# Kernel optimization log

Hardware: AMD Instinct MI355X
Metric: run time of the kernel (lower is better)

Reference implementation:

```python
import jax, jax.numpy as jnp
import numpy as np

B, H, W, D = 4, 64, 64, 384
M, P = 12, 9
DH = D // M             # 32 head dim
DFF = 3 * D             # 1152 FFN hidden
N = H * W               # 4096 queries (single level)


def setup_inputs():
    key = jax.random.key(0)
    ks = jax.random.split(key, 12)
    g = lambda k, s, sc=0.02: jax.random.normal(k, s, jnp.float32) * sc
    return {
        "x": jax.random.normal(ks[0], (B, D, H, W), jnp.float32),
        "qry_masks": jnp.zeros((B, H, W), jnp.float32),
        "so_w": g(ks[1], (M * P * 2, D)), "so_b": g(ks[2], (M * P * 2,)),
        "aw_w": g(ks[3], (M * P, D)), "aw_b": g(ks[4], (M * P,)),
        "vp_w": g(ks[5], (D, D)), "vp_b": jnp.zeros((D,), jnp.float32),
        "op_w": g(ks[6], (D, D)), "op_b": jnp.zeros((D,), jnp.float32),
        "ln1_g": jnp.ones((D,), jnp.float32), "ln1_b": jnp.zeros((D,), jnp.float32),
        "w1": g(ks[7], (DFF, D)), "w2": g(ks[8], (D, DFF)),
        "ln2_g": jnp.ones((D,), jnp.float32), "ln2_b": jnp.zeros((D,), jnp.float32),
        "level_embed": g(ks[9], (1, D), 1.0),
    }


def _layernorm(x, g, b, eps=1e-5):
    mu = x.mean(-1, keepdims=True)
    v = ((x - mu) ** 2).mean(-1, keepdims=True)
    return (x - mu) * jax.lax.rsqrt(v + eps) * g + b


def _sine_pos(mask):
    # mask: [B,H,W] bool. mmdet SinePositionalEncoding(num_feats=D//2, normalize=True)
    not_mask = (~mask).astype(jnp.float32)
    y = jnp.cumsum(not_mask, 1)
    x = jnp.cumsum(not_mask, 2)
    eps, scale = 1e-6, 2.0 * np.pi
    y = y / (y[:, -1:, :] + eps) * scale
    x = x / (x[:, :, -1:] + eps) * scale
    nf = D // 2
    dim_t = 10000.0 ** (2.0 * (jnp.arange(nf) // 2).astype(jnp.float32) / nf)
    px, py = x[..., None] / dim_t, y[..., None] / dim_t

    def interleave(p):
        return jnp.stack([jnp.sin(p[..., 0::2]), jnp.cos(p[..., 1::2])], -1).reshape(p.shape[:-1] + (nf,))

    return jnp.concatenate([interleave(py), interleave(px)], -1)  # [B,H,W,D]


def _bilinear_gather(v, px, py):
    # v: [B,M,HW,DH]; px,py: [B,M,NP] pixel coords (grid_sample align_corners=False, zero pad)
    x0 = jnp.floor(px); y0 = jnp.floor(py)
    lx, ly = px - x0, py - y0
    x0i, y0i = x0.astype(jnp.int32), y0.astype(jnp.int32)
    out = jnp.zeros(v.shape[:2] + (px.shape[-1], v.shape[-1]), v.dtype)
    for dx, dy, wgt in ((0, 0, (1 - lx) * (1 - ly)), (1, 0, lx * (1 - ly)),
                        (0, 1, (1 - lx) * ly), (1, 1, lx * ly)):
        xi, yi = x0i + dx, y0i + dy
        valid = ((xi >= 0) & (xi < W) & (yi >= 0) & (yi < H)).astype(v.dtype)
        idx = jnp.clip(yi, 0, H - 1) * W + jnp.clip(xi, 0, W - 1)
        g = jnp.take_along_axis(v, idx[..., None], axis=2)  # [B,M,NP,DH]
        out = out + (wgt * valid)[..., None] * g
    return out


def _msdeform_attn(q, value_in, ref, mask_flat,
                   so_w, so_b, aw_w, aw_b, vp_w, vp_b, op_w, op_b):
    value = value_in @ vp_w.T + vp_b                      # [B,N,D]
    value = jnp.where(mask_flat[..., None], 0.0, value)
    so = (q @ so_w.T + so_b).reshape(B, N, M, P, 2)       # single level
    aw = jax.nn.softmax((q @ aw_w.T + aw_b).reshape(B, N, M, P), axis=-1)
    norm = jnp.array([W, H], jnp.float32)
    loc = ref[:, :, None, None, :] + so / norm            # [B,N,M,P,2] in [0,1]
    v = value.reshape(B, N, M, DH).transpose(0, 2, 1, 3)  # [B,M,HW,DH]
    px = (loc[..., 0] * W - 0.5).transpose(0, 2, 1, 3).reshape(B, M, N * P)
    py = (loc[..., 1] * H - 0.5).transpose(0, 2, 1, 3).reshape(B, M, N * P)
    sampled = _bilinear_gather(v, px, py).reshape(B, M, N, P, DH)
    out = jnp.einsum('bmnpd,bnmp->bnmd', sampled, aw).reshape(B, N, D)
    return out @ op_w.T + op_b


def reference(x, qry_masks, so_w, so_b, aw_w, aw_b, vp_w, vp_b, op_w, op_b,
              ln1_g, ln1_b, w1, w2, ln2_g, ln2_b, level_embed):
    mask = (qry_masks == 255.0)                           # [B,H,W] bool
    pos = _sine_pos(mask).reshape(B, N, D) + level_embed[0]
    src = x.reshape(B, D, N).transpose(0, 2, 1)           # [B,N,D]
    mask_flat = mask.reshape(B, N)
    gy, gx = jnp.meshgrid((jnp.arange(H, dtype=jnp.float32) + 0.5) / H,
                          (jnp.arange(W, dtype=jnp.float32) + 0.5) / W, indexing='ij')
    ref = jnp.stack([gx.reshape(-1), gy.reshape(-1)], -1)[None]  # [1,N,2] (x,y)
    q = src
    attn = _msdeform_attn(q + pos, q, ref, mask_flat,
                          so_w, so_b, aw_w, aw_b, vp_w, vp_b, op_w, op_b)
    q = _layernorm(q + attn, ln1_g, ln1_b)
    q = _layernorm(q + jax.nn.relu(q @ w1.T) @ w2.T, ln2_g, ln2_b)
    return q.transpose(0, 2, 1).reshape(B, D, H, W)
```

## Files before the change

kernel.cpp:

```cpp
#include <hip/hip_runtime.h>
#include <math.h>

#define Bc   4
#define Hc   64
#define Wc   64
#define Dc   384
#define Nc   4096
#define Mc   12
#define Pc   9
#define DHc  32
#define DFFc 1152
#define BNc  (Bc*Nc)

typedef __attribute__((ext_vector_type(8))) short short8;
typedef __attribute__((ext_vector_type(4))) float floatx4;

__device__ __forceinline__ ushort f2bf(float f) {
    union { float f; unsigned u; } v; v.f = f;
    unsigned r = v.u + 0x7fffu + ((v.u >> 16) & 1u);
    return (ushort)(r >> 16);
}
__device__ __forceinline__ float bf2f(ushort u) {
    union { unsigned u; float f; } v; v.u = (unsigned)u << 16; return v.f;
}

__device__ __forceinline__ void gload_lds16(const void* g, void* l) {
    __builtin_amdgcn_global_load_lds(
        (const __attribute__((address_space(1))) void*)(uintptr_t)g,
        (__attribute__((address_space(3))) void*)(uintptr_t)l,
        16, 0, 0);
}

#define SOW_N  82944
#define AWW_N  41472
#define VPW_N  147456
#define OPW_N  147456
#define W1_N   442368
#define W2_N   442368
#define WTOT   1304064

__global__ void init_kernel(const float* __restrict__ so_w,
                            const float* __restrict__ aw_w,
                            const float* __restrict__ vp_w,
                            const float* __restrict__ op_w,
                            const float* __restrict__ w1,
                            const float* __restrict__ w2,
                            const float* __restrict__ so_b,
                            const float* __restrict__ aw_b,
                            const float* __restrict__ qmask,
                            ushort* __restrict__ out,
                            float* __restrict__ bias_out,
                            float* __restrict__ cum_y,
                            float* __restrict__ cum_x) {
    int i = blockIdx.x * 256 + threadIdx.x;
    if (i < WTOT) {
        float v;
        int j = i;
        if (j < SOW_N) v = so_w[j];
        else if ((j -= SOW_N) < AWW_N) v = aw_w[j];
        else if ((j -= AWW_N) < VPW_N) v = vp_w[j];
        else if ((j -= VPW_N) < OPW_N) v = op_w[j];
        else if ((j -= OPW_N) < W1_N)  v = w1[j];
        else { j -= W1_N; v = w2[j]; }
        out[i] = f2bf(v);
        return;
    }
    int j = i - WTOT;
    if (j < 384) {
        bias_out[j] = (j < 216) ? so_b[j] : (j < 324 ? aw_b[j - 216] : 0.f);
        return;
    }
    int t = j - 384;
    if (t < Bc * Wc) {
        int b = t / Wc, w = t % Wc;
        float run = 0.f;
        for (int h = 0; h < Hc; ++h) {
            run += (qmask[(b * Hc + h) * Wc + w] == 255.0f) ? 0.f : 1.f;
            cum_y[(b * Hc + h) * Wc + w] = run;
        }
    } else if (t < Bc * Wc + Bc * Hc) {
        int t2 = t - Bc * Wc;
        int b = t2 / Hc, h = t2 % Hc;
        float run = 0.f;
        for (int w = 0; w < Wc; ++w) {
            run += (qmask[(b * Hc + h) * Wc + w] == 255.0f) ? 0.f : 1.f;
            cum_x[(b * Hc + h) * Wc + w] = run;
        }
    }
}

__global__ void transpose_pos_kernel(const float* __restrict__ x,
                                     const float* __restrict__ cum_y,
                                     const float* __restrict__ cum_x,
                                     const float* __restrict__ level_embed,
                                     ushort* __restrict__ src_bf,
                                     ushort* __restrict__ qpos_bf) {
    __shared__ float tile[32][33];
    int b  = blockIdx.z;
    int n0 = blockIdx.x * 32, d0 = blockIdx.y * 32;
    int tx = threadIdx.x, ty = threadIdx.y;
    tile[ty][tx] = x[((size_t)b * Dc + (d0 + ty)) * Nc + (n0 + tx)];
    __syncthreads();
    int n = n0 + ty, d = d0 + tx;
    float v = tile[tx][ty];
    size_t oi = ((size_t)b * Nc + n) * Dc + d;
    src_bf[oi] = f2bf(v);
    int h = n >> 6, w = n & 63;
    const float TWO_PI = 6.28318530717958647692f;
    float vy = cum_y[(b * Hc + h) * Wc + w] /
               (cum_y[(b * Hc + (Hc - 1)) * Wc + w] + 1e-6f) * TWO_PI;
    float vx = cum_x[(b * Hc + h) * Wc + w] /
               (cum_x[(b * Hc + h) * Wc + (Wc - 1)] + 1e-6f) * TWO_PI;
    int   i  = (d < 192) ? d : d - 192;
    float vv = (d < 192) ? vy : vx;
    float e   = (float)(i >> 1) * (2.0f / 192.0f);
    float idt = exp2f(e * -13.28771237954945f);
    float ang = vv * idt;
    float pe  = (i & 1) ? __cosf(ang) : __sinf(ang);
    qpos_bf[oi] = f2bf(v + pe + level_embed[d]);
}

template <int KT>
__device__ __forceinline__ void gemm_core(
        const ushort* __restrict__ A, const ushort* __restrict__ Wt,
        const float* __restrict__ bias,
        float* __restrict__ Cf, ushort* __restrict__ Cb,
        int Nout, int relu, const float* __restrict__ qmask,
        ushort* As, ushort* Bs) {
    constexpr int NCH = KT / 32;
    const int tid  = threadIdx.x;
    const int m0   = blockIdx.x * 128;
    const int n0   = blockIdx.y * 128;
    const int lane = tid & 63;
    const int wv   = tid >> 6;
    const int wr   = (wv >> 1) * 64;
    const int wc   = (wv & 1) * 64;
    const int quad = lane >> 4;
    const int lrow = lane & 15;
    const int srow = wv * 32 + (lane >> 2);
    const int scol = (lane & 3) * 8;

    floatx4 acc[4][4];
    #pragma unroll
    for (int i = 0; i < 4; ++i)
        #pragma unroll
        for (int j = 0; j < 4; ++j)
            acc[i][j] = (floatx4)(0.f);

    #pragma unroll
    for (int s = 0; s < 2; ++s) {
        gload_lds16(A  + (size_t)(m0 + srow + s * 16) * KT + scol,
                    As + wv * 1024 + s * 512);
        gload_lds16(Wt + (size_t)(n0 + srow + s * 16) * KT + scol,
                    Bs + wv * 1024 + s * 512);
    }

    for (int c = 0; c < NCH; ++c) {
        const int cur = c & 1;
        __syncthreads();
        if (c + 1 < NCH) {
            const int k0 = (c + 1) * 32;
            #pragma unroll
            for (int s = 0; s < 2; ++s) {
                gload_lds16(A  + (size_t)(m0 + srow + s * 16) * KT + k0 + scol,
                            As + (cur ^ 1) * 4096 + wv * 1024 + s * 512);
                gload_lds16(Wt + (size_t)(n0 + srow + s * 16) * KT + k0 + scol,
                            Bs + (cur ^ 1) * 4096 + wv * 1024 + s * 512);
            }
        }
        short8 afr[4], bfr[4];
        #pragma unroll
        for (int i = 0; i < 4; ++i)
            afr[i] = *(const short8*)(As + cur * 4096 +
                                      (wr + i * 16 + lrow) * 32 + quad * 8);
        #pragma unroll
        for (int j = 0; j < 4; ++j)
            bfr[j] = *(const short8*)(Bs + cur * 4096 +
                                      (wc + j * 16 + lrow) * 32 + quad * 8);
        #pragma unroll
        for (int i = 0; i < 4; ++i)
            #pragma unroll
            for (int j = 0; j < 4; ++j)
                acc[i][j] = __builtin_amdgcn_mfma_f32_16x16x32_bf16(
                    afr[i], bfr[j], acc[i][j], 0, 0, 0);
    }

    float mz[4][4];
    #pragma unroll
    for (int i = 0; i < 4; ++i)
        #pragma unroll
        for (int r = 0; r < 4; ++r) {
            int row = m0 + wr + i * 16 + quad * 4 + r;
            mz[i][r] = (qmask && qmask[row] == 255.0f) ? 0.f : 1.f;
        }

    #pragma unroll
    for (int i = 0; i < 4; ++i) {
        #pragma unroll
        for (int j = 0; j < 4; ++j) {
            int col = n0 + wc + j * 16 + lrow;
            if (col >= Nout) continue;
            float bsv = bias ? bias[col] : 0.f;
            #pragma unroll
            for (int r = 0; r < 4; ++r) {
                int row = m0 + wr + i * 16 + quad * 4 + r;
                float v = acc[i][j][r] + bsv;
                if (relu) v = fmaxf(v, 0.f);
                v *= mz[i][r];
                if (Cf) Cf[(size_t)row * Nout + col] = v;
                if (Cb) Cb[(size_t)row * Nout + col] = f2bf(v);
            }
        }
    }
}

template <int KT>
__global__ __launch_bounds__(256) void gemm_single_kernel(
        const ushort* __restrict__ A, const ushort* __restrict__ Wt,
        const float* __restrict__ bias,
        float* __restrict__ Cf, ushort* __restrict__ Cb,
        int Nout, int relu, const float* __restrict__ qmask) {
    __shared__ ushort As[2 * 128 * 32];
    __shared__ ushort Bs[2 * 128 * 32];
    gemm_core<KT>(A, Wt, bias, Cf, Cb, Nout, relu, qmask, As, Bs);
}

__global__ __launch_bounds__(256) void gemm_dual_kernel(
        const ushort* __restrict__ A0, const ushort* __restrict__ W0,
        const float* __restrict__ b0, float* __restrict__ Cf0,
        const ushort* __restrict__ A1, const ushort* __restrict__ W1,
        const float* __restrict__ b1, ushort* __restrict__ Cb1,
        const float* __restrict__ qmask) {
    __shared__ ushort As[2 * 128 * 32];
    __shared__ ushort Bs[2 * 128 * 32];
    if (blockIdx.z == 0)
        gemm_core<384>(A0, W0, b0, Cf0, nullptr, 384, 0, nullptr, As, Bs);
    else
        gemm_core<384>(A1, W1, b1, nullptr, Cb1, 384, 0, qmask, As, Bs);
}

template <int KT, int MODE>
__global__ __launch_bounds__(512, 2) void gemm_fullrow_kernel(
        const ushort* __restrict__ A, const ushort* __restrict__ Wt,
        const float* __restrict__ bias, const void* __restrict__ resid,
        const float* __restrict__ g, const float* __restrict__ beta,
        float* __restrict__ outf, ushort* __restrict__ outb) {
    constexpr int NCH = KT / 32;
    __shared__ ushort Bs[8 * 3 * 1536];
    __shared__ float eps1[8][64], eps2[8][64];
    __shared__ float mu_l[64], rs_l[64];
    const int tid  = threadIdx.x;
    const int lane = tid & 63;
    const int wv   = tid >> 6;
    const int quad = lane >> 4;
    const int lrow = lane & 15;
    const int m0   = blockIdx.x * 64;
    const int srow = lane >> 2;
    const int scol = (lane & 3) * 8;

    ushort* BsW = Bs + wv * (3 * 1536);
    const ushort* wsrc  = Wt + (size_t)(wv * 48 + srow) * KT + scol;
    const ushort* abase = A  + (size_t)(m0 + lrow) * KT + quad * 8;

    floatx4 acc[4][3];
    #pragma unroll
    for (int i = 0; i < 4; ++i)
        #pragma unroll
        for (int j = 0; j < 3; ++j)
            acc[i][j] = (floatx4)(0.f);

#define STAGE_W(c, buf)                                                      \
    gload_lds16(wsrc + (size_t)0 * 16 * KT + (c) * 32, BsW + (buf) * 1536);  \
    gload_lds16(wsrc + (size_t)1 * 16 * KT + (c) * 32, BsW + (buf) * 1536 + 512); \
    gload_lds16(wsrc + (size_t)2 * 16 * KT + (c) * 32, BsW + (buf) * 1536 + 1024);

#define LOAD_A(dst, c)                                                       \
    dst[0] = *(const short8*)(abase + (size_t)0 * 16 * KT + (c) * 32);       \
    dst[1] = *(const short8*)(abase + (size_t)1 * 16 * KT + (c) * 32);       \
    dst[2] = *(const short8*)(abase + (size_t)2 * 16 * KT + (c) * 32);       \
    dst[3] = *(const short8*)(abase + (size_t)3 * 16 * KT + (c) * 32);

#define DO_MFMA(afr, buf)                                                    \
    {   short8 bfr[3];                                                       \
        bfr[0] = *(const short8*)(BsW + (buf) * 1536 + (lrow)      * 32 + quad * 8); \
        bfr[1] = *(const short8*)(BsW + (buf) * 1536 + (16 + lrow) * 32 + quad * 8); \
        bfr[2] = *(const short8*)(BsW + (buf) * 1536 + (32 + lrow) * 32 + quad * 8); \
        _Pragma("unroll")                                                    \
        for (int i_ = 0; i_ < 4; ++i_) {                                     \
            acc[i_][0] = __builtin_amdgcn_mfma_f32_16x16x32_bf16(afr[i_], bfr[0], acc[i_][0], 0, 0, 0); \
            acc[i_][1] = __builtin_amdgcn_mfma_f32_16x16x32_bf16(afr[i_], bfr[1], acc[i_][1], 0, 0, 0); \
            acc[i_][2] = __builtin_amdgcn_mfma_f32_16x16x32_bf16(afr[i_], bfr[2], acc[i_][2], 0, 0, 0); \
        } }

    short8 afrC[4], afrN[4];
    LOAD_A(afrC, 0)
    STAGE_W(0, 0)
    STAGE_W(1, 1)

    for (int c = 0; c < NCH - 1; ++c) {
        asm volatile("s_waitcnt vmcnt(3)" ::: "memory");
        LOAD_A(afrN, c + 1)
        if (c + 2 < NCH) { STAGE_W(c + 2, (c + 2) % 3) }
        DO_MFMA(afrC, c % 3)
        #pragma unroll
        for (int i = 0; i < 4; ++i) afrC[i] = afrN[i];
    }
    asm volatile("s_waitcnt vmcnt(0)" ::: "memory");
    DO_MFMA(afrC, (NCH - 1) % 3)

#undef STAGE_W
#undef LOAD_A
#undef DO_MFMA

    float s1[16], s2[16];
    #pragma unroll
    for (int k = 0; k < 16; ++k) { s1[k] = 0.f; s2[k] = 0.f; }
    #pragma unroll
    for (int i = 0; i < 4; ++i) {
        #pragma unroll
        for (int r = 0; r < 4; ++r) {
            int rl = i * 16 + quad * 4 + r;
            #pragma unroll
            for (int j = 0; j < 3; ++j) {
                int col = wv * 48 + j * 16 + lrow;
                float t = acc[i][j][r];
                if (bias) t += bias[col];
                if (MODE == 0)
                    t += bf2f(((const ushort*)resid)[(size_t)(m0 + rl) * Dc + col]);
                else
                    t += ((const float*)resid)[(size_t)(m0 + rl) * Dc + col];
                acc[i][j][r] = t;
                s1[i * 4 + r] += t;
                s2[i * 4 + r] += t * t;
            }
        }
    }
    #pragma unroll
    for (int mm = 1; mm < 16; mm <<= 1) {
        #pragma unroll
        for (int k = 0; k < 16; ++k) {
            s1[k] += __shfl_xor(s1[k], mm);
            s2[k] += __shfl_xor(s2[k], mm);
        }
    }
    if (lrow == 0) {
        #pragma unroll
        for (int i = 0; i < 4; ++i)
            #pragma unroll
            for (int r = 0; r < 4; ++r) {
                int rl = i * 16 + quad * 4 + r;
                eps1[wv][rl] = s1[i * 4 + r];
                eps2[wv][rl] = s2[i * 4 + r];
            }
    }
    __syncthreads();
    if (tid < 64) {
        float a1 = 0.f, a2 = 0.f;
        #pragma unroll
        for (int w = 0; w < 8; ++w) { a1 += eps1[w][tid]; a2 += eps2[w][tid]; }
        float mu  = a1 * (1.0f / Dc);
        float var = a2 * (1.0f / Dc) - mu * mu;
        mu_l[tid] = mu;
        rs_l[tid] = rsqrtf(var + 1e-5f);
    }
    __syncthreads();

    #pragma unroll
    for (int i = 0; i < 4; ++i) {
        #pragma unroll
        for (int r = 0; r < 4; ++r) {
            int rl = i * 16 + quad * 4 + r;
            float mu = mu_l[rl], rs = rs_l[rl];
            #pragma unroll
            for (int j = 0; j < 3; ++j) {
                int col = wv * 48 + j * 16 + lrow;
                acc[i][j][r] = (acc[i][j][r] - mu) * rs * g[col] + beta[col];
            }
        }
    }

    if (MODE == 0) {
        #pragma unroll
        for (int i = 0; i < 4; ++i)
            #pragma unroll
            for (int j = 0; j < 3; ++j) {
                int col = wv * 48 + j * 16 + lrow;
                #pragma unroll
                for (int r = 0; r < 4; ++r) {
                    int rl = i * 16 + quad * 4 + r;
                    float v = acc[i][j][r];
                    outf[(size_t)(m0 + rl) * Dc + col] = v;
                    outb[(size_t)(m0 + rl) * Dc + col] = f2bf(v);
                }
            }
    } else {
        float* tile = (float*)Bs;
        const int b   = m0 >> 12;
        const int n0r = m0 & 4095;
        #pragma unroll
        for (int gp = 0; gp < 2; ++gp) {
            __syncthreads();
            if ((wv >> 2) == gp) {
                int cbase = (wv & 3) * 48;
                #pragma unroll
                for (int i = 0; i < 4; ++i)
                    #pragma unroll
                    for (int j = 0; j < 3; ++j) {
                        int c = cbase + j * 16 + lrow;
                        #pragma unroll
                        for (int r = 0; r < 4; ++r) {
                            int rl = i * 16 + quad * 4 + r;
                            tile[rl * 193 + c] = acc[i][j][r];
                        }
                    }
            }
            __syncthreads();
            const int row = tid & 63;
            const int cp  = tid >> 6;
            #pragma unroll
            for (int it = 0; it < 24; ++it) {
                int c = it * 8 + cp;
                outf[((size_t)(b * Dc + gp * 192 + c)) * Nc + n0r + row] =
                    tile[row * 193 + c];
            }
        }
    }
}

__global__ __launch_bounds__(256) void deform_attn_kernel(
        const ushort* __restrict__ value_bf, const float* __restrict__ soaw,
        ushort* __restrict__ out) {
    int bid   = blockIdx.x;
    int slice = bid % 48;
    int h     = bid / 48;
    int m  = slice % Mc;
    int b  = slice / Mc;
    int w  = threadIdx.x >> 2;
    int l4 = threadIdx.x & 3;
    int n  = (h << 6) | w;
    int bn = b * Nc + n;
    const float* sop = soaw + (size_t)bn * 384 + m * 18;
    const float* lgt = soaw + (size_t)bn * 384 + 216 + m * Pc;
    float awv[Pc];
    float mx = lgt[0];
    #pragma unroll
    for (int i = 1; i < Pc; ++i) mx = fmaxf(mx, lgt[i]);
    float ssum = 0.f;
    #pragma unroll
    for (int i = 0; i < Pc; ++i) { awv[i] = __expf(lgt[i] - mx); ssum += awv[i]; }
    float sinv = 1.f / ssum;
    const ushort* vb = value_bf + ((size_t)b * Nc) * Dc + m * DHc + l4 * 8;
    float acc[8] = {0.f, 0.f, 0.f, 0.f, 0.f, 0.f, 0.f, 0.f};
    #pragma unroll
    for (int p = 0; p < Pc; ++p) {
        float2 so2 = *(const float2*)(sop + p * 2);
        float px = (float)w + so2.x;
        float py = (float)h + so2.y;
        float x0f = floorf(px), y0f = floorf(py);
        float lx = px - x0f, ly = py - y0f;
        int x0 = (int)x0f, y0 = (int)y0f;
        int x1 = x0 + 1,  y1 = y0 + 1;
        float a = awv[p] * sinv;
        float w00 = (1.f - lx) * (1.f - ly) * a;
        float w01 = lx * (1.f - ly) * a;
        float w10 = (1.f - lx) * ly * a;
        float w11 = lx * ly * a;
        bool bx0 = (unsigned)x0 < 64u, bx1 = (unsigned)x1 < 64u;
        bool by0 = (unsigned)y0 < 64u, by1 = (unsigned)y1 < 64u;
        w00 = (bx0 && by0) ? w00 : 0.f;
        w01 = (bx1 && by0) ? w01 : 0.f;
        w10 = (bx0 && by1) ? w10 : 0.f;
        w11 = (bx1 && by1) ? w11 : 0.f;
        int cx0 = min(max(x0, 0), 63), cx1 = min(max(x1, 0), 63);
        int cy0 = min(max(y0, 0), 63), cy1 = min(max(y1, 0), 63);
        uint4 q00 = *(const uint4*)(vb + (size_t)(cy0 * 64 + cx0) * Dc);
        uint4 q01 = *(const uint4*)(vb + (size_t)(cy0 * 64 + cx1) * Dc);
        uint4 q10 = *(const uint4*)(vb + (size_t)(cy1 * 64 + cx0) * Dc);
        uint4 q11 = *(const uint4*)(vb + (size_t)(cy1 * 64 + cx1) * Dc);
        union { unsigned u; float f; } t;
        #define ACC2(word, wg, k)                                   \
            t.u = (word) << 16;         acc[k]     += (wg) * t.f;   \
            t.u = (word) & 0xffff0000u; acc[k + 1] += (wg) * t.f;
        #define ACC8(q, wg) \
            ACC2((q).x, wg, 0) ACC2((q).y, wg, 2) ACC2((q).z, wg, 4) ACC2((q).w, wg, 6)
        ACC8(q00, w00) ACC8(q01, w01) ACC8(q10, w10) ACC8(q11, w11)
        #undef ACC8
        #undef ACC2
    }
    short8 o;
    #pragma unroll
    for (int k = 0; k < 8; ++k) o[k] = (short)f2bf(acc[k]);
    *(short8*)(out + (size_t)bn * Dc + m * DHc + l4 * 8) = o;
}

extern "C" void kernel_launch(void* const* d_in, const int* in_sizes, int n_in,
                              void* d_out, int out_size, void* d_ws, size_t ws_size,
                              hipStream_t stream) {
    (void)in_sizes; (void)n_in; (void)out_size; (void)ws_size;
    const float* x      = (const float*)d_in[0];
    const float* qmask  = (const float*)d_in[1];
    const float* so_w   = (const float*)d_in[2];
    const float* so_b   = (const float*)d_in[3];
    const float* aw_w   = (const float*)d_in[4];
    const float* aw_b   = (const float*)d_in[5];
    const float* vp_w   = (const float*)d_in[6];
    const float* vp_b   = (const float*)d_in[7];
    const float* op_w   = (const float*)d_in[8];
    const float* op_b   = (const float*)d_in[9];
    const float* ln1_g  = (const float*)d_in[10];
    const float* ln1_b  = (const float*)d_in[11];
    const float* w1     = (const float*)d_in[12];
    const float* w2     = (const float*)d_in[13];
    const float* ln2_g  = (const float*)d_in[14];
    const float* ln2_b  = (const float*)d_in[15];
    const float* lvl    = (const float*)d_in[16];
    float* out = (float*)d_out;

    float*  ws       = (float*)d_ws;
    float*  q1_f     = ws;
    ushort* src_bf   = (ushort*)(q1_f + 6291456);
    ushort* qpos_bf  = src_bf + 6291456;
    ushort* value_bf = qpos_bf + 6291456;
    ushort* hbuf_bf  = value_bf + 6291456;
    float*  soaw_f   = (float*)hbuf_bf;
    ushort* wbuf     = hbuf_bf + 18874368;
    float*  soaw_bias= (float*)(wbuf + 1304064);
    float*  cum_y    = soaw_bias + 384;
    float*  cum_x    = cum_y + 16384;

    const ushort* soaw_wb = wbuf;
    const ushort* vp_wb = soaw_wb + SOW_N + AWW_N;
    const ushort* op_wb = vp_wb + VPW_N;
    const ushort* w1_b  = op_wb + OPW_N;
    const ushort* w2_b  = w1_b + W1_N;

    init_kernel<<<(WTOT + 384 + 512 + 255) / 256, 256, 0, stream>>>(
        so_w, aw_w, vp_w, op_w, w1, w2, so_b, aw_b, qmask,
        wbuf, soaw_bias, cum_y, cum_x);
    transpose_pos_kernel<<<dim3(Nc / 32, Dc / 32, Bc), dim3(32, 32), 0, stream>>>(
        x, cum_y, cum_x, lvl, src_bf, qpos_bf);
    gemm_dual_kernel<<<dim3(BNc / 128, 3, 2), 256, 0, stream>>>(
        qpos_bf, soaw_wb, soaw_bias, soaw_f,
        src_bf, vp_wb, vp_b, value_bf, qmask);
    deform_attn_kernel<<<3072, 256, 0, stream>>>(
        value_bf, soaw_f, qpos_bf);
    gemm_fullrow_kernel<384, 0><<<BNc / 64, 512, 0, stream>>>(
        qpos_bf, op_wb, op_b, src_bf, ln1_g, ln1_b, q1_f, qpos_bf);
    gemm_single_kernel<384><<<dim3(BNc / 128, 9), 256, 0, stream>>>(
        qpos_bf, w1_b, nullptr, nullptr, hbuf_bf, DFFc, 1, nullptr);
    gemm_fullrow_kernel<1152, 1><<<BNc / 64, 512, 0, stream>>>(
        hbuf_bf, w2_b, nullptr, q1_f, ln2_g, ln2_b, out, nullptr);
}
```

Baseline: 292.9 us.

## Deepen A-fragment prefetch to four register slots in GEMM main loop

Restructures the GEMM K-loop so A fragments are prefetched three chunks ahead into a four-slot register ring, and W tiles stay triple-buffered in LDS. The loop is fully unrolled with adjusted vmcnt waits, so more global loads are in flight and register copies between iterations go away. The cost is more VGPRs held for A fragments, which could lower occupancy. The hand-counted vmcnt values must match the real load order.

New measurement: 319.4 us. +9.1%, slower.

```diff
diff --git a/kernel.cpp b/kernel.cpp
--- a/kernel.cpp
+++ b/kernel.cpp
@@ -274,39 +274,42 @@
     gload_lds16(wsrc + (size_t)1 * 16 * KT + (c) * 32, BsW + (buf) * 1536 + 512); \
     gload_lds16(wsrc + (size_t)2 * 16 * KT + (c) * 32, BsW + (buf) * 1536 + 1024);
 
-#define LOAD_A(dst, c)                                                       \
-    dst[0] = *(const short8*)(abase + (size_t)0 * 16 * KT + (c) * 32);       \
-    dst[1] = *(const short8*)(abase + (size_t)1 * 16 * KT + (c) * 32);       \
-    dst[2] = *(const short8*)(abase + (size_t)2 * 16 * KT + (c) * 32);       \
-    dst[3] = *(const short8*)(abase + (size_t)3 * 16 * KT + (c) * 32);
-
-#define DO_MFMA(afr, buf)                                                    \
+#define LOAD_A(slot, c)                                                      \
+    afr[slot][0] = *(const short8*)(abase + (size_t)0 * 16 * KT + (c) * 32); \
+    afr[slot][1] = *(const short8*)(abase + (size_t)1 * 16 * KT + (c) * 32); \
+    afr[slot][2] = *(const short8*)(abase + (size_t)2 * 16 * KT + (c) * 32); \
+    afr[slot][3] = *(const short8*)(abase + (size_t)3 * 16 * KT + (c) * 32);
+
+#define DO_MFMA(slot, buf)                                                   \
     {   short8 bfr[3];                                                       \
         bfr[0] = *(const short8*)(BsW + (buf) * 1536 + (lrow)      * 32 + quad * 8); \
         bfr[1] = *(const short8*)(BsW + (buf) * 1536 + (16 + lrow) * 32 + quad * 8); \
         bfr[2] = *(const short8*)(BsW + (buf) * 1536 + (32 + lrow) * 32 + quad * 8); \
         _Pragma("unroll")                                                    \
         for (int i_ = 0; i_ < 4; ++i_) {                                     \
-            acc[i_][0] = __builtin_amdgcn_mfma_f32_16x16x32_bf16(afr[i_], bfr[0], acc[i_][0], 0, 0, 0); \
-            acc[i_][1] = __builtin_amdgcn_mfma_f32_16x16x32_bf16(afr[i_], bfr[1], acc[i_][1], 0, 0, 0); \
-            acc[i_][2] = __builtin_amdgcn_mfma_f32_16x16x32_bf16(afr[i_], bfr[2], acc[i_][2], 0, 0, 0); \
+            acc[i_][0] = __builtin_amdgcn_mfma_f32_16x16x32_bf16(afr[slot][i_], bfr[0], acc[i_][0], 0, 0, 0); \
+            acc[i_][1] = __builtin_amdgcn_mfma_f32_16x16x32_bf16(afr[slot][i_], bfr[1], acc[i_][1], 0, 0, 0); \
+            acc[i_][2] = __builtin_amdgcn_mfma_f32_16x16x32_bf16(afr[slot][i_], bfr[2], acc[i_][2], 0, 0, 0); \
         } }
 
-    short8 afrC[4], afrN[4];
-    LOAD_A(afrC, 0)
+    short8 afr[4][4];
+    LOAD_A(0, 0)
     STAGE_W(0, 0)
+    LOAD_A(1, 1)
     STAGE_W(1, 1)
-
-    for (int c = 0; c < NCH - 1; ++c) {
-        asm volatile("s_waitcnt vmcnt(3)" ::: "memory");
-        LOAD_A(afrN, c + 1)
-        if (c + 2 < NCH) { STAGE_W(c + 2, (c + 2) % 3) }
-        DO_MFMA(afrC, c % 3)
-        #pragma unroll
-        for (int i = 0; i < 4; ++i) afrC[i] = afrN[i];
-    }
+    LOAD_A(2, 2)
+
+    #pragma unroll
+    for (int c = 0; c <= NCH - 3; ++c) {
+        asm volatile("s_waitcnt vmcnt(11)" ::: "memory");
+        STAGE_W(c + 2, (c + 2) % 3)
+        if (c + 3 < NCH) { LOAD_A((c + 3) % 4, c + 3) }
+        DO_MFMA(c % 4, c % 3)
+    }
+    asm volatile("s_waitcnt vmcnt(7)" ::: "memory");
+    DO_MFMA((NCH - 2) % 4, (NCH - 2) % 3)
     asm volatile("s_waitcnt vmcnt(0)" ::: "memory");
-    DO_MFMA(afrC, (NCH - 1) % 3)
+    DO_MFMA((NCH - 1) % 4, (NCH - 1) % 3)
 
 #undef STAGE_W
 #undef LOAD_A
```
